# Performance work log

Hardware: AMD Instinct MI355X
Metric: run time of the kernel (lower is better)

## Reference

```python
import jax, jax.numpy as jnp
import numpy as np
from functools import partial

N_NODES = 50000


def gcn_conv(x, row, col, norm, W, b, num_nodes):
    # x: [N, Fin], W: [Fout, Fin] (torch Linear weight layout), b: [Fout]
    h = x @ W.T                                   # [N, Fout]
    msg = norm[:, None] * h[row]                  # per-edge message, gather x_j = x[row]
    out = jax.ops.segment_sum(msg, col, num_segments=num_nodes)  # scatter-add to target col
    return out + b


def _build_norm(row, col, edge_weight, num_nodes):
    # add self-loops with weight 1.0
    loops = jnp.arange(num_nodes, dtype=row.dtype)
    row_f = jnp.concatenate([row, loops])
    col_f = jnp.concatenate([col, loops])
    ew_f = jnp.concatenate([edge_weight, jnp.ones((num_nodes,), edge_weight.dtype)])
    # degree counts occurrences of row (unweighted, like PyG degree())
    deg = jax.ops.segment_sum(jnp.ones_like(ew_f), row_f, num_segments=num_nodes)
    dinv = jnp.where(deg > 0, deg ** -0.5, 0.0).astype(edge_weight.dtype)
    norm = dinv[row_f] * ew_f * dinv[col_f]
    return row_f, col_f, norm


def setup_inputs() -> dict:
    key = jax.random.key(0)
    k = jax.random.split(key, 8)
    N, E = N_NODES, 800000
    Fin, H, C = 256, 96, 40
    x = jax.random.normal(k[0], (N, Fin), dtype=jnp.float32)
    edge_index = jax.random.randint(k[1], (2, E), 0, N, dtype=jnp.int64)
    edge_weight = jax.random.uniform(k[2], (E,), dtype=jnp.float32)
    W1 = jax.random.normal(k[3], (H, Fin), dtype=jnp.float32) * (1.0 / np.sqrt(Fin))
    b1 = jnp.zeros((H,), jnp.float32)
    W2 = jax.random.normal(k[4], (C, H), dtype=jnp.float32) * (1.0 / np.sqrt(H))
    b2 = jnp.zeros((C,), jnp.float32)
    return {"x": x, "edge_index": edge_index, "edge_weight": edge_weight,
            "W1": W1, "b1": b1, "W2": W2, "b2": b2}


def reference(x, edge_index, edge_weight, W1, b1, W2, b2):
    N = x.shape[0]
    row, col = edge_index[0], edge_index[1]
    row_f, col_f, norm = _build_norm(row, col, edge_weight, N)
    h = jax.nn.relu(gcn_conv(x, row_f, col_f, norm, W1, b1, N))
    # dropout is identity in eval mode
    out = gcn_conv(h, row_f, col_f, norm, W2, b2, N)
    return jax.nn.log_softmax(out, axis=1)
```

## Files before the change

### kernel.cpp

```cpp
#include <hip/hip_runtime.h>
#include <hip/hip_bf16.h>
#include <hip/hip_fp16.h>
#include <math.h>

#define NN 50000
#define EE 800000
#define FIN 256
#define FH 96
#define FC 40
#define NBK 196

typedef _Float16 h4 __attribute__((ext_vector_type(4)));
typedef _Float16 h8 __attribute__((ext_vector_type(8)));
typedef float f32x4 __attribute__((ext_vector_type(4)));

__device__ __forceinline__ unsigned pack_edge(int row, float w) {
    _Float16 he = (_Float16)w;
    unsigned short us;
    __builtin_memcpy(&us, &he, 2);
    return (unsigned)row | ((unsigned)us << 16);
}
__device__ __forceinline__ float unpack_w(unsigned pk) {
    unsigned short us = (unsigned short)(pk >> 16);
    _Float16 hv;
    __builtin_memcpy(&hv, &us, 2);
    return (float)hv;
}


#define G1B 782

__global__ __launch_bounds__(256) void k_fused1(const float* __restrict__ x,
                                                const float* __restrict__ W,
                                                _Float16* __restrict__ g0h,
                                                const int* __restrict__ ei, int E,
                                                unsigned* __restrict__ copies,
                                                unsigned* __restrict__ bcnt2d, int n) {
    __shared__ unsigned lds[12500];
    int bid = blockIdx.x;
    int tid = threadIdx.x;

    if (bid < G1B) {
        _Float16* xsp = (_Float16*)lds;
        _Float16* wsp = xsp + 64 * 72;
        int row0 = bid * 64;
        int l = tid & 63, w = tid >> 6;
        int l15 = l & 15, lg = l >> 4;

        f32x4 acc[6];
#pragma unroll
        for (int c = 0; c < 6; ++c) acc[c] = (f32x4)0.f;

        for (int kc = 0; kc < 4; ++kc) {
            int kbase = kc * 64;
#pragma unroll
            for (int i = 0; i < 4; ++i) {
                int it = tid + 256 * i;
                int r = it >> 4, k4 = it & 15;
                float4 v = make_float4(0.f, 0.f, 0.f, 0.f);
                int gr = row0 + r;
                if (gr < n) v = *(const float4*)&x[gr * FIN + kbase + k4 * 4];
                h4 hv = {(_Float16)v.x, (_Float16)v.y, (_Float16)v.z, (_Float16)v.w};
                *(h4*)&xsp[r * 72 + k4 * 4] = hv;
            }
#pragma unroll
            for (int i = 0; i < 6; ++i) {
                int it = tid + 256 * i;
                int r = it >> 4, k4 = it & 15;
                float4 v = *(const float4*)&W[r * FIN + kbase + k4 * 4];
                h4 hv = {(_Float16)v.x, (_Float16)v.y, (_Float16)v.z, (_Float16)v.w};
                *(h4*)&wsp[r * 72 + k4 * 4] = hv;
            }
            __syncthreads();
#pragma unroll
            for (int ks = 0; ks < 2; ++ks) {
                h8 a = *(const h8*)&xsp[(16 * w + l15) * 72 + ks * 32 + lg * 8];
#pragma unroll
                for (int ct = 0; ct < 6; ++ct) {
                    h8 b = *(const h8*)&wsp[(ct * 16 + l15) * 72 + ks * 32 + lg * 8];
                    acc[ct] = __builtin_amdgcn_mfma_f32_16x16x32_f16(a, b, acc[ct], 0, 0, 0);
                }
            }
            __syncthreads();
        }
#pragma unroll
        for (int r = 0; r < 4; ++r) {
            int grow = row0 + 16 * w + lg * 4 + r;
            if (grow < n) {
#pragma unroll
                for (int ct = 0; ct < 6; ++ct)
                    g0h[(size_t)grow * FH + ct * 16 + l15] = (_Float16)acc[ct][r];
            }
        }
    } else if (bid < 910) {
        int b2 = bid - G1B;
        int slice = b2 & 63, half = b2 >> 6;
        int ES = (E + 63) >> 6;
        const int* ptr = ei;
        for (int i = tid; i < 12500; i += 256) lds[i] = 0u;
        __syncthreads();
        int lo = slice * ES, hi = min(lo + ES, E);
        int nlo = half * 25000;
        for (int i = lo + tid; i < hi; i += 256) {
            int rel = ptr[i] - nlo;
            if ((unsigned)rel < 25000u)
                atomicAdd(&lds[rel >> 1], 1u << ((rel & 1) << 4));
        }
        __syncthreads();
        unsigned* dst = copies + (size_t)(half * 64 + slice) * 12500;
        for (int i = tid; i < 12500; i += 256) dst[i] = lds[i];
    } else {
        int chunk = bid - 910;
        int ES = (E + 63) >> 6;
        const int* col = ei + E;
        for (int i = tid; i < NBK; i += 256) lds[i] = 0u;
        __syncthreads();
        int lo = chunk * ES, hi = min(lo + ES, E);
        for (int i = lo + tid; i < hi; i += 256) atomicAdd(&lds[col[i] >> 8], 1u);
        __syncthreads();
        for (int i = tid; i < NBK; i += 256) bcnt2d[chunk * 256 + i] = lds[i];
    }
}


__global__ __launch_bounds__(256) void k_reduce(const unsigned* __restrict__ copies,
                                                const unsigned* __restrict__ bcnt2d,
                                                float* __restrict__ dinv,
                                                unsigned* __restrict__ bstart,
                                                unsigned* __restrict__ gcur,
                                                unsigned* __restrict__ off, unsigned E) {
    int t = blockIdx.x * blockDim.x + threadIdx.x;
    if (t < 25000) {
        int half = t / 12500, w = t - half * 12500;
        unsigned sr = 0;
        const unsigned* br = copies + (size_t)half * 64 * 12500 + w;
#pragma unroll 8
        for (int s = 0; s < 64; ++s) sr += br[s * 12500];
        int n0 = half * 25000 + 2 * w;
        dinv[n0]     = rsqrtf((float)((sr & 0xffffu) + 1u));
        dinv[n0 + 1] = rsqrtf((float)((sr >> 16) + 1u));
    }
    if (blockIdx.x == 0) {
        __shared__ unsigned sb[256];
        int tt = threadIdx.x;
        unsigned v = 0;
        if (tt < NBK) {
#pragma unroll 8
            for (int c = 0; c < 64; ++c) v += bcnt2d[c * 256 + tt];
        }
        sb[tt] = v;
        __syncthreads();
        for (int o = 1; o < 256; o <<= 1) {
            unsigned tv = (tt >= o) ? sb[tt - o] : 0u;
            __syncthreads();
            sb[tt] += tv;
            __syncthreads();
        }
        if (tt < NBK) {
            unsigned ex = sb[tt] - v;
            bstart[tt] = ex;
            gcur[tt] = ex;
            bstart[tt + 1] = sb[tt];
        }
        if (tt == 0) off[NN] = E;
    }
}


__global__ __launch_bounds__(256) void k_bucket(const int* __restrict__ row,
                                                const int* __restrict__ col,
                                                const float* __restrict__ ew,
                                                const float* __restrict__ dinv,
                                                unsigned* __restrict__ gcur,
                                                unsigned* __restrict__ bkc,
                                                unsigned* __restrict__ bkpk, int E) {
    __shared__ unsigned cnt[NBK];
    __shared__ unsigned cur[NBK];
    int tid = threadIdx.x;
    int CH = (E + gridDim.x - 1) / gridDim.x;
    int lo = blockIdx.x * CH, hi = min(lo + CH, E);
    for (int i = tid; i < NBK; i += 256) cnt[i] = 0u;
    __syncthreads();
    for (int i = lo + tid; i < hi; i += 256) atomicAdd(&cnt[col[i] >> 8], 1u);
    __syncthreads();
    for (int i = tid; i < NBK; i += 256) cur[i] = atomicAdd(&gcur[i], cnt[i]);
    __syncthreads();
    for (int i = lo + tid; i < hi; i += 256) {
        int c = col[i];
        int r = row[i];
        unsigned pos = atomicAdd(&cur[c >> 8], 1u);
        bkc[pos] = (unsigned)c;
        bkpk[pos] = pack_edge(r, dinv[r] * ew[i]);
    }
}


__global__ __launch_bounds__(256) void k_place(const unsigned* __restrict__ bkc,
                                               const unsigned* __restrict__ bkpk,
                                               const unsigned* __restrict__ bstart,
                                               unsigned* __restrict__ off,
                                               unsigned* __restrict__ epk, int n) {
    __shared__ unsigned cnt[256];
    __shared__ unsigned cur[256];
    int b = blockIdx.x;
    int tid = threadIdx.x;
    int node0 = b * 256;
    unsigned st = bstart[b], en = bstart[b + 1];
    cnt[tid] = 0u;
    __syncthreads();
    for (unsigned i = st + tid; i < en; i += 256) atomicAdd(&cnt[bkc[i] & 255], 1u);
    __syncthreads();
    unsigned v = cnt[tid];
    cur[tid] = v;
    __syncthreads();
    for (int o = 1; o < 256; o <<= 1) {
        unsigned tv = (tid >= o) ? cur[tid - o] : 0u;
        __syncthreads();
        cur[tid] += tv;
        __syncthreads();
    }
    unsigned base = st + cur[tid] - v;
    int node = node0 + tid;
    if (node < n) off[node] = base;
    cur[tid] = base;
    __syncthreads();
    for (unsigned i = st + tid; i < en; i += 256) {
        unsigned c = bkc[i];
        unsigned pos = atomicAdd(&cur[c & 255], 1u);
        epk[pos] = bkpk[i];
    }
}


__global__ __launch_bounds__(256) void k_agg96(const _Float16* __restrict__ g0h,
                                               const unsigned* __restrict__ off,
                                               const unsigned* __restrict__ epk,
                                               const float* __restrict__ dinv,
                                               const float* __restrict__ b,
                                               _Float16* __restrict__ outh, int n) {
    int tid = blockIdx.x * 256 + threadIdx.x;
    int node = tid / 12;
    int f8 = tid - node * 12;
    if (node >= n) return;
    float s = dinv[node];
    const h8* gp = (const h8*)g0h;
    h8 self = gp[(size_t)node * 12 + f8];
    float acc[8];
#pragma unroll
    for (int j = 0; j < 8; ++j) acc[j] = s * (float)self[j];
    unsigned st = off[node], en = off[node + 1];
    unsigned e = st;
    for (; e + 8 <= en; e += 8) {
        unsigned k0 = epk[e + 0], k1 = epk[e + 1], k2 = epk[e + 2], k3 = epk[e + 3];
        unsigned k4 = epk[e + 4], k5 = epk[e + 5], k6 = epk[e + 6], k7 = epk[e + 7];
        h8 ga = gp[(size_t)(k0 & 0xffffu) * 12 + f8];
        h8 gb = gp[(size_t)(k1 & 0xffffu) * 12 + f8];
        h8 gc = gp[(size_t)(k2 & 0xffffu) * 12 + f8];
        h8 gd = gp[(size_t)(k3 & 0xffffu) * 12 + f8];
        h8 ge = gp[(size_t)(k4 & 0xffffu) * 12 + f8];
        h8 gf = gp[(size_t)(k5 & 0xffffu) * 12 + f8];
        h8 gg = gp[(size_t)(k6 & 0xffffu) * 12 + f8];
        h8 gh = gp[(size_t)(k7 & 0xffffu) * 12 + f8];
        float w0 = unpack_w(k0), w1 = unpack_w(k1), w2 = unpack_w(k2), w3 = unpack_w(k3);
        float w4 = unpack_w(k4), w5 = unpack_w(k5), w6 = unpack_w(k6), w7 = unpack_w(k7);
#pragma unroll
        for (int j = 0; j < 8; ++j) acc[j] = fmaf(w0, (float)ga[j], acc[j]);
#pragma unroll
        for (int j = 0; j < 8; ++j) acc[j] = fmaf(w1, (float)gb[j], acc[j]);
#pragma unroll
        for (int j = 0; j < 8; ++j) acc[j] = fmaf(w2, (float)gc[j], acc[j]);
#pragma unroll
        for (int j = 0; j < 8; ++j) acc[j] = fmaf(w3, (float)gd[j], acc[j]);
#pragma unroll
        for (int j = 0; j < 8; ++j) acc[j] = fmaf(w4, (float)ge[j], acc[j]);
#pragma unroll
        for (int j = 0; j < 8; ++j) acc[j] = fmaf(w5, (float)gf[j], acc[j]);
#pragma unroll
        for (int j = 0; j < 8; ++j) acc[j] = fmaf(w6, (float)gg[j], acc[j]);
#pragma unroll
        for (int j = 0; j < 8; ++j) acc[j] = fmaf(w7, (float)gh[j], acc[j]);
    }
    for (; e + 4 <= en; e += 4) {
        unsigned k0 = epk[e + 0], k1 = epk[e + 1], k2 = epk[e + 2], k3 = epk[e + 3];
        h8 ga = gp[(size_t)(k0 & 0xffffu) * 12 + f8];
        h8 gb = gp[(size_t)(k1 & 0xffffu) * 12 + f8];
        h8 gc = gp[(size_t)(k2 & 0xffffu) * 12 + f8];
        h8 gd = gp[(size_t)(k3 & 0xffffu) * 12 + f8];
        float w0 = unpack_w(k0), w1 = unpack_w(k1), w2 = unpack_w(k2), w3 = unpack_w(k3);
#pragma unroll
        for (int j = 0; j < 8; ++j) acc[j] = fmaf(w0, (float)ga[j], acc[j]);
#pragma unroll
        for (int j = 0; j < 8; ++j) acc[j] = fmaf(w1, (float)gb[j], acc[j]);
#pragma unroll
        for (int j = 0; j < 8; ++j) acc[j] = fmaf(w2, (float)gc[j], acc[j]);
#pragma unroll
        for (int j = 0; j < 8; ++j) acc[j] = fmaf(w3, (float)gd[j], acc[j]);
    }
    for (; e < en; ++e) {
        unsigned k = epk[e];
        h8 g = gp[(size_t)(k & 0xffffu) * 12 + f8];
        float wv = unpack_w(k);
#pragma unroll
        for (int j = 0; j < 8; ++j) acc[j] = fmaf(wv, (float)g[j], acc[j]);
    }
    float4 bv0 = ((const float4*)b)[f8 * 2];
    float4 bv1 = ((const float4*)b)[f8 * 2 + 1];
    const float bb[8] = {bv0.x, bv0.y, bv0.z, bv0.w, bv1.x, bv1.y, bv1.z, bv1.w};
    h8 o;
#pragma unroll
    for (int j = 0; j < 8; ++j) o[j] = (_Float16)fmaxf(fmaf(s, acc[j], bb[j]), 0.f);
    *(h8*)&outh[(size_t)node * FH + f8 * 8] = o;
}


__global__ __launch_bounds__(256) void k_gemm2(const _Float16* __restrict__ h,
                                               const float* __restrict__ W2,
                                               _Float16* __restrict__ g1h, int n) {
    __shared__ _Float16 hs[64][104];
    __shared__ _Float16 wsm[48][104];
    int tid = threadIdx.x;
    int row0 = blockIdx.x * 64;
    int l = tid & 63, w = tid >> 6;
    int l15 = l & 15, lg = l >> 4;

    f32x4 acc[3];
#pragma unroll
    for (int c = 0; c < 3; ++c) acc[c] = (f32x4)0.f;

#pragma unroll
    for (int i = 0; i < 6; ++i) {
        int it = tid + 256 * i;
        int r = it / 24, k4 = it - r * 24;
        int gr = row0 + r;
        h4 hv = {(_Float16)0.f, (_Float16)0.f, (_Float16)0.f, (_Float16)0.f};
        if (gr < n) hv = *(const h4*)&h[(size_t)gr * FH + k4 * 4];
        *(h4*)&hs[r][k4 * 4] = hv;
    }
#pragma unroll
    for (int i = 0; i < 5; ++i) {
        int it = tid + 256 * i;
        if (it < 1152) {
            int r = it / 24, k4 = it - r * 24;
            h4 hv = {(_Float16)0.f, (_Float16)0.f, (_Float16)0.f, (_Float16)0.f};
            if (r < FC) {
                float4 v = *(const float4*)&W2[r * FH + k4 * 4];
                hv[0] = (_Float16)v.x; hv[1] = (_Float16)v.y;
                hv[2] = (_Float16)v.z; hv[3] = (_Float16)v.w;
            }
            *(h4*)&wsm[r][k4 * 4] = hv;
        }
    }
    __syncthreads();
#pragma unroll
    for (int ks = 0; ks < 3; ++ks) {
        h8 a = *(const h8*)&hs[16 * w + l15][ks * 32 + lg * 8];
#pragma unroll
        for (int ct = 0; ct < 3; ++ct) {
            h8 b = *(const h8*)&wsm[ct * 16 + l15][ks * 32 + lg * 8];
            acc[ct] = __builtin_amdgcn_mfma_f32_16x16x32_f16(a, b, acc[ct], 0, 0, 0);
        }
    }
#pragma unroll
    for (int r = 0; r < 4; ++r) {
        int grow = row0 + 16 * w + lg * 4 + r;
        if (grow < n) {
#pragma unroll
            for (int ct = 0; ct < 3; ++ct) {
                int colc = ct * 16 + l15;
                if (colc < FC)
                    g1h[(size_t)grow * FC + colc] = (_Float16)acc[ct][r];
            }
        }
    }
}


__global__ __launch_bounds__(256) void k_agg40lsm(const _Float16* __restrict__ g1h,
                                                  const unsigned* __restrict__ off,
                                                  const unsigned* __restrict__ epk,
                                                  const float* __restrict__ dinv,
                                                  const float* __restrict__ b,
                                                  float* __restrict__ out, int n) {
    __shared__ float sm[50][41];
    int tid = threadIdx.x;
    int ln = tid / 5;
    int f8 = tid - ln * 5;
    int node = blockIdx.x * 50 + ln;
    bool active = (tid < 250) && (node < n);
    float acc[8];
#pragma unroll
    for (int j = 0; j < 8; ++j) acc[j] = 0.f;
    if (active) {
        float s = dinv[node];
        const h8* gp = (const h8*)g1h;
        h8 self = gp[(size_t)node * 5 + f8];
#pragma unroll
        for (int j = 0; j < 8; ++j) acc[j] = s * (float)self[j];
        unsigned st = off[node], en = off[node + 1];
        unsigned e = st;
        for (; e + 4 <= en; e += 4) {
            unsigned k0 = epk[e + 0], k1 = epk[e + 1], k2 = epk[e + 2], k3 = epk[e + 3];
            h8 ga = gp[(size_t)(k0 & 0xffffu) * 5 + f8];
            h8 gb = gp[(size_t)(k1 & 0xffffu) * 5 + f8];
            h8 gc = gp[(size_t)(k2 & 0xffffu) * 5 + f8];
            h8 gd = gp[(size_t)(k3 & 0xffffu) * 5 + f8];
            float w0 = unpack_w(k0), w1 = unpack_w(k1), w2 = unpack_w(k2), w3 = unpack_w(k3);
#pragma unroll
            for (int j = 0; j < 8; ++j) acc[j] = fmaf(w0, (float)ga[j], acc[j]);
#pragma unroll
            for (int j = 0; j < 8; ++j) acc[j] = fmaf(w1, (float)gb[j], acc[j]);
#pragma unroll
            for (int j = 0; j < 8; ++j) acc[j] = fmaf(w2, (float)gc[j], acc[j]);
#pragma unroll
            for (int j = 0; j < 8; ++j) acc[j] = fmaf(w3, (float)gd[j], acc[j]);
        }
        for (; e < en; ++e) {
            unsigned k = epk[e];
            h8 g = gp[(size_t)(k & 0xffffu) * 5 + f8];
            float wv = unpack_w(k);
#pragma unroll
            for (int j = 0; j < 8; ++j) acc[j] = fmaf(wv, (float)g[j], acc[j]);
        }
        float4 bv0 = ((const float4*)b)[f8 * 2];
        float4 bv1 = ((const float4*)b)[f8 * 2 + 1];
        const float bb[8] = {bv0.x, bv0.y, bv0.z, bv0.w, bv1.x, bv1.y, bv1.z, bv1.w};
#pragma unroll
        for (int j = 0; j < 8; ++j) {
            acc[j] = fmaf(s, acc[j], bb[j]);
            sm[ln][f8 * 8 + j] = acc[j];
        }
    }
    __syncthreads();
    if (tid < 50) {
        int nd = blockIdx.x * 50 + tid;
        if (nd < n) {
            float m = -INFINITY;
#pragma unroll 8
            for (int j = 0; j < FC; ++j) m = fmaxf(m, sm[tid][j]);
            float sum = 0.f;
#pragma unroll 8
            for (int j = 0; j < FC; ++j) sum += expf(sm[tid][j] - m);
            sm[tid][40] = logf(sum) + m;
        }
    }
    __syncthreads();
    if (active) {
        float lse = sm[ln][40];
        float4 o0 = make_float4(acc[0] - lse, acc[1] - lse, acc[2] - lse, acc[3] - lse);
        float4 o1 = make_float4(acc[4] - lse, acc[5] - lse, acc[6] - lse, acc[7] - lse);
        *(float4*)&out[(size_t)node * FC + f8 * 8] = o0;
        *(float4*)&out[(size_t)node * FC + f8 * 8 + 4] = o1;
    }
}


extern "C" void kernel_launch(void* const* d_in, const int* in_sizes, int n_in,
                              void* d_out, int out_size, void* d_ws, size_t ws_size,
                              hipStream_t stream) {
    const float* x  = (const float*)d_in[0];
    const int*   ei = (const int*)d_in[1];
    const float* ew = (const float*)d_in[2];
    const float* W1 = (const float*)d_in[3];
    const float* b1 = (const float*)d_in[4];
    const float* W2 = (const float*)d_in[5];
    const float* b2 = (const float*)d_in[6];
    float* out = (float*)d_out;

    const int N = NN;
    const int E = in_sizes[1] / 2;
    const int* row = ei;
    const int* col = ei + E;

    float* ws = (float*)d_ws;
    float*    dinv   = (float*)(ws + 0);
    unsigned* off    = (unsigned*)(ws + 50176);
    unsigned* bcnt2d = (unsigned*)(ws + 100480);
    unsigned* bstart = (unsigned*)(ws + 116864);
    unsigned* gcur   = (unsigned*)(ws + 117120);
    unsigned* copies = (unsigned*)(ws + 150976);
    unsigned* bkc    = (unsigned*)(ws + 150976);
    unsigned* bkpk   = (unsigned*)(ws + 950976);
    _Float16* h      = (_Float16*)(ws + 150976);
    unsigned* epk    = (unsigned*)(ws + 4950976);
    _Float16* g0h    = (_Float16*)(ws + 6550976);
    _Float16* g1h    = (_Float16*)(ws + 8950976);

    const int B = 256;

    hipLaunchKernelGGL(k_fused1, dim3(974), dim3(B), 0, stream,
                       x, W1, g0h, ei, E, copies, bcnt2d, N);
    hipLaunchKernelGGL(k_reduce, dim3(98), dim3(B), 0, stream,
                       copies, bcnt2d, dinv, bstart, gcur, off, (unsigned)E);

    hipLaunchKernelGGL(k_bucket, dim3(320), dim3(B), 0, stream,
                       row, col, ew, dinv, gcur, bkc, bkpk, E);
    hipLaunchKernelGGL(k_place, dim3(NBK), dim3(B), 0, stream, bkc, bkpk, bstart, off, epk, N);

    hipLaunchKernelGGL(k_agg96, dim3((N * 12 + B - 1) / B), dim3(B), 0, stream,
                       g0h, off, epk, dinv, b1, h, N);

    hipLaunchKernelGGL(k_gemm2, dim3((N + 63) / 64), dim3(B), 0, stream, h, W2, g1h, N);

    hipLaunchKernelGGL(k_agg40lsm, dim3((N + 49) / 50), dim3(B), 0, stream,
                       g1h, off, epk, dinv, b2, out, N);
}
```

Measured before the change: 130.6 us.

## Prefetch GEMM tiles into registers and quarter the degree histogram LDS

The first-layer GEMM blocks now load the next K-chunk of x and W into registers while the current chunk is converted and written to shared memory. This overlaps global load latency with the compute loop. The degree histogram is split into 4 node quarters with 32 edge slices each instead of 2 halves with 64 slices, which halves the LDS array to 6250 words. Less LDS per block should raise occupancy for every block type in the fused kernel, and the reduction now sums 32 copies instead of 64. The register prefetch adds VGPR pressure, and each histogram block now reads twice as many edges.

```diff
diff --git a/kernel.cpp b/kernel.cpp
--- a/kernel.cpp
+++ b/kernel.cpp
@@ -36,7 +36,7 @@
                                                 const int* __restrict__ ei, int E,
                                                 unsigned* __restrict__ copies,
                                                 unsigned* __restrict__ bcnt2d, int n) {
-    __shared__ unsigned lds[12500];
+    __shared__ unsigned lds[6250];
     int bid = blockIdx.x;
     int tid = threadIdx.x;
 
@@ -51,25 +51,54 @@
 #pragma unroll
         for (int c = 0; c < 6; ++c) acc[c] = (f32x4)0.f;
 
-        for (int kc = 0; kc < 4; ++kc) {
-            int kbase = kc * 64;
+        float4 px[4], pw[6];
+        {
 #pragma unroll
             for (int i = 0; i < 4; ++i) {
                 int it = tid + 256 * i;
                 int r = it >> 4, k4 = it & 15;
-                float4 v = make_float4(0.f, 0.f, 0.f, 0.f);
                 int gr = row0 + r;
-                if (gr < n) v = *(const float4*)&x[gr * FIN + kbase + k4 * 4];
-                h4 hv = {(_Float16)v.x, (_Float16)v.y, (_Float16)v.z, (_Float16)v.w};
-                *(h4*)&xsp[r * 72 + k4 * 4] = hv;
+                px[i] = make_float4(0.f, 0.f, 0.f, 0.f);
+                if (gr < n) px[i] = *(const float4*)&x[gr * FIN + k4 * 4];
             }
 #pragma unroll
             for (int i = 0; i < 6; ++i) {
                 int it = tid + 256 * i;
                 int r = it >> 4, k4 = it & 15;
-                float4 v = *(const float4*)&W[r * FIN + kbase + k4 * 4];
-                h4 hv = {(_Float16)v.x, (_Float16)v.y, (_Float16)v.z, (_Float16)v.w};
+                pw[i] = *(const float4*)&W[r * FIN + k4 * 4];
+            }
+        }
+        for (int kc = 0; kc < 4; ++kc) {
+#pragma unroll
+            for (int i = 0; i < 4; ++i) {
+                int it = tid + 256 * i;
+                int r = it >> 4, k4 = it & 15;
+                h4 hv = {(_Float16)px[i].x, (_Float16)px[i].y, (_Float16)px[i].z, (_Float16)px[i].w};
+                *(h4*)&xsp[r * 72 + k4 * 4] = hv;
+            }
+#pragma unroll
+            for (int i = 0; i < 6; ++i) {
+                int it = tid + 256 * i;
+                int r = it >> 4, k4 = it & 15;
+                h4 hv = {(_Float16)pw[i].x, (_Float16)pw[i].y, (_Float16)pw[i].z, (_Float16)pw[i].w};
                 *(h4*)&wsp[r * 72 + k4 * 4] = hv;
+            }
+            if (kc < 3) {
+                int kbase = (kc + 1) * 64;
+#pragma unroll
+                for (int i = 0; i < 4; ++i) {
+                    int it = tid + 256 * i;
+                    int r = it >> 4, k4 = it & 15;
+                    int gr = row0 + r;
+                    px[i] = make_float4(0.f, 0.f, 0.f, 0.f);
+                    if (gr < n) px[i] = *(const float4*)&x[gr * FIN + kbase + k4 * 4];
+                }
+#pragma unroll
+                for (int i = 0; i < 6; ++i) {
+                    int it = tid + 256 * i;
+                    int r = it >> 4, k4 = it & 15;
+                    pw[i] = *(const float4*)&W[r * FIN + kbase + k4 * 4];
+                }
             }
             __syncthreads();
 #pragma unroll
@@ -94,21 +123,22 @@
         }
     } else if (bid < 910) {
         int b2 = bid - G1B;
-        int slice = b2 & 63, half = b2 >> 6;
-        int ES = (E + 63) >> 6;
+        int q = b2 >> 5;
+        int slice = b2 & 31;
+        int ES2 = (E + 31) >> 5;
         const int* ptr = ei;
-        for (int i = tid; i < 12500; i += 256) lds[i] = 0u;
-        __syncthreads();
-        int lo = slice * ES, hi = min(lo + ES, E);
-        int nlo = half * 25000;
+        for (int i = tid; i < 6250; i += 256) lds[i] = 0u;
+        __syncthreads();
+        int lo = slice * ES2, hi = min(lo + ES2, E);
+        int nlo = q * 12500;
         for (int i = lo + tid; i < hi; i += 256) {
             int rel = ptr[i] - nlo;
-            if ((unsigned)rel < 25000u)
+            if ((unsigned)rel < 12500u)
                 atomicAdd(&lds[rel >> 1], 1u << ((rel & 1) << 4));
         }
         __syncthreads();
-        unsigned* dst = copies + (size_t)(half * 64 + slice) * 12500;
-        for (int i = tid; i < 12500; i += 256) dst[i] = lds[i];
+        unsigned* dst = copies + (size_t)b2 * 6250;
+        for (int i = tid; i < 6250; i += 256) dst[i] = lds[i];
     } else {
         int chunk = bid - 910;
         int ES = (E + 63) >> 6;
@@ -131,12 +161,12 @@
                                                 unsigned* __restrict__ off, unsigned E) {
     int t = blockIdx.x * blockDim.x + threadIdx.x;
     if (t < 25000) {
-        int half = t / 12500, w = t - half * 12500;
+        int quarter = t / 6250, w = t - quarter * 6250;
         unsigned sr = 0;
-        const unsigned* br = copies + (size_t)half * 64 * 12500 + w;
+        const unsigned* br = copies + (size_t)(quarter * 32) * 6250 + w;
 #pragma unroll 8
-        for (int s = 0; s < 64; ++s) sr += br[s * 12500];
-        int n0 = half * 25000 + 2 * w;
+        for (int s = 0; s < 32; ++s) sr += br[s * 6250];
+        int n0 = quarter * 12500 + 2 * w;
         dinv[n0]     = rsqrtf((float)((sr & 0xffffu) + 1u));
         dinv[n0 + 1] = rsqrtf((float)((sr >> 16) + 1u));
     }
```

New measurement: 136.4 us. 1.04x slower.
